# Performance work log

Hardware: AMD Instinct MI355X
Metric: run time of the kernel (lower is better)

Reference implementation:

```python
import jax, jax.numpy as jnp
import numpy as np

N = 50000          # num nodes
E = 800000         # num edges (avg degree 16)
R = 8              # num relations
IN = 128
H0 = 256
H1 = 64


def _w(key, shape, fan_in):
    return jax.random.normal(key, shape, dtype=jnp.float32) * (1.0 / np.sqrt(fan_in))


def setup_inputs() -> dict:
    key = jax.random.key(0)
    ks = jax.random.split(key, 16)
    x = jax.random.normal(ks[0], (N, IN), dtype=jnp.float32)
    edge_index = jax.random.randint(ks[1], (2, E), 0, N, dtype=jnp.int64)
    edge_type = jax.random.randint(ks[2], (E,), 0, R, dtype=jnp.int64)
    return {
        "x": x,
        "edge_index": edge_index,
        "edge_type": edge_type,
        # RGCNConv params: per-relation weights [R, in, out], root weight [in, out], bias [out]
        "W1": _w(ks[3], (R, IN, H0), IN), "root1": _w(ks[4], (IN, H0), IN), "b1": jnp.zeros((H0,), jnp.float32),
        "W2": _w(ks[5], (R, H0, H0), H0), "root2": _w(ks[6], (H0, H0), H0), "b2": jnp.zeros((H0,), jnp.float32),
        "W3": _w(ks[7], (R, H0, H0), H0), "root3": _w(ks[8], (H0, H0), H0), "b3": jnp.zeros((H0,), jnp.float32),
        "W4": _w(ks[9], (R, H0, H1), H0), "root4": _w(ks[10], (H0, H1), H0), "b4": jnp.zeros((H1,), jnp.float32),
    }


def rgcn_layer(x, edge_index, edge_type, W, root, bias):
    """PyG RGCNConv: out_i = x_i @ root + sum_r (1/|N_r(i)|) sum_{j in N_r(i)} x_j @ W_r + bias.
    Aggregation is linear, so aggregate source features per (relation, dst) first,
    then apply the R small GEMMs — avoids per-edge [E, out] message materialization."""
    src, dst = edge_index[0], edge_index[1]
    seg = edge_type * N + dst                      # combined (relation, dst) segment id
    nseg = R * N
    agg = jax.ops.segment_sum(x[src], seg, num_segments=nseg)          # [R*N, in]
    cnt = jax.ops.segment_sum(jnp.ones((seg.shape[0],), x.dtype), seg, num_segments=nseg)
    agg = agg / jnp.maximum(cnt, 1.0)[:, None]                          # mean per (r, i)
    agg = agg.reshape(R, N, x.shape[1])                                 # [R, N, in]
    return jnp.einsum('rni,rio->no', agg, W) + x @ root + bias


def reference(x, edge_index, edge_type, W1, root1, b1, W2, root2, b2, W3, root3, b3, W4, root4, b4):
    h = jax.nn.relu(rgcn_layer(x, edge_index, edge_type, W1, root1, b1))
    h = jax.nn.relu(rgcn_layer(h, edge_index, edge_type, W2, root2, b2))
    h = jax.nn.relu(rgcn_layer(h, edge_index, edge_type, W3, root3, b3))
    return rgcn_layer(h, edge_index, edge_type, W4, root4, b4)
```

## Files before the change

### kernel.cpp

```cpp
#include <hip/hip_runtime.h>

#define N_NODES 50000
#define N_PAD   50048
#define N_EDGES 800000
#define N_REL   8
#define NSEG    (N_REL * N_NODES)
#define SCAN_NB 391
#define NSTRIPE 391
#define SPX     49

typedef short bf16x8 __attribute__((ext_vector_type(8)));
typedef float f32x4  __attribute__((ext_vector_type(4)));

__device__ __forceinline__ ushort f2bf(float f) {
    union { float f; unsigned u; } c; c.f = f;
    unsigned u = c.u + 0x7fffu + ((c.u >> 16) & 1u);
    return (ushort)(u >> 16);
}
__device__ __forceinline__ void add8(float* s, uint4 v) {
    unsigned u[4] = {v.x, v.y, v.z, v.w};
    #pragma unroll
    for (int k = 0; k < 4; ++k) {
        s[2 * k]     += __uint_as_float(u[k] << 16);
        s[2 * k + 1] += __uint_as_float(u[k] & 0xffff0000u);
    }
}
__device__ __forceinline__ void fma8(float* s, uint4 v, float w) {
    unsigned u[4] = {v.x, v.y, v.z, v.w};
    #pragma unroll
    for (int k = 0; k < 4; ++k) {
        s[2 * k]     = fmaf(__uint_as_float(u[k] << 16),        w, s[2 * k]);
        s[2 * k + 1] = fmaf(__uint_as_float(u[k] & 0xffff0000u), w, s[2 * k + 1]);
    }
}
__device__ __forceinline__ void async16(const ushort* g, ushort* l) {
    __builtin_amdgcn_global_load_lds((const __attribute__((address_space(1))) void*)g,
                                     (__attribute__((address_space(3))) void*)l, 16, 0, 0);
}


__global__ void count_edges(const int* __restrict__ dst, const int* __restrict__ et,
                            int* __restrict__ cnt) {
    int e = blockIdx.x * 256 + threadIdx.x;
    if (e < N_EDGES) atomicAdd(&cnt[dst[e] * N_REL + et[e]], 1);
}

__global__ __launch_bounds__(256) void scan_pass1(const int* __restrict__ cnt,
                                                  int* __restrict__ sums) {
    __shared__ int sc[256];
    int b = blockIdx.x, t = threadIdx.x;
    int base = b * 1024 + t * 4;
    int v = 0;
    #pragma unroll
    for (int i = 0; i < 4; ++i) { int idx = base + i; if (idx < NSEG) v += cnt[idx]; }
    sc[t] = v; __syncthreads();
    for (int off = 1; off < 256; off <<= 1) {
        int x = (t >= off) ? sc[t - off] : 0;
        __syncthreads(); sc[t] += x; __syncthreads();
    }
    if (t == 255) sums[b] = sc[255];
}

__global__ __launch_bounds__(512) void scan_pass2(int* __restrict__ sums, int nb) {
    __shared__ int sc[512];
    int t = threadIdx.x;
    int v = (t < nb) ? sums[t] : 0;
    sc[t] = v; __syncthreads();
    for (int off = 1; off < 512; off <<= 1) {
        int x = (t >= off) ? sc[t - off] : 0;
        __syncthreads(); sc[t] += x; __syncthreads();
    }
    if (t < nb) sums[t] = sc[t] - v;
}

__global__ __launch_bounds__(256) void scan_pass3(const int* __restrict__ cnt,
                                                  const int* __restrict__ sums,
                                                  int* __restrict__ row_ptr) {
    __shared__ int sc[256];
    int b = blockIdx.x, t = threadIdx.x;
    int base = b * 1024 + t * 4;
    int e[4]; int v = 0;
    #pragma unroll
    for (int i = 0; i < 4; ++i) { int idx = base + i; e[i] = (idx < NSEG) ? cnt[idx] : 0; v += e[i]; }
    sc[t] = v; __syncthreads();
    for (int off = 1; off < 256; off <<= 1) {
        int x = (t >= off) ? sc[t - off] : 0;
        __syncthreads(); sc[t] += x; __syncthreads();
    }
    int run = sums[b] + (sc[t] - v);
    #pragma unroll
    for (int i = 0; i < 4; ++i) {
        int idx = base + i;
        if (idx < NSEG) row_ptr[idx] = run;
        run += e[i];
    }
    if (b == 0 && t == 0) row_ptr[NSEG] = N_EDGES;
}

__global__ void place_edges(const int* __restrict__ src, const int* __restrict__ dst,
                            const int* __restrict__ et, const int* __restrict__ row_ptr,
                            int* __restrict__ cnt, int* __restrict__ sorted) {
    int e = blockIdx.x * 256 + threadIdx.x;
    if (e >= N_EDGES) return;
    int r = et[e];
    int key = dst[e] * N_REL + r;
    int old = atomicSub(&cnt[key], 1);
    int r0 = row_ptr[key];
    int c = row_ptr[key + 1] - r0;
    sorted[r0 + old - 1] = src[e] | (r << 17) | (c << 20);
}


__global__ void convert_weights(const float* __restrict__ W, const float* __restrict__ root,
                                ushort* __restrict__ BT, int K, int O, int NPAD) {
    int idx = blockIdx.x * 256 + threadIdx.x;
    if (idx >= NPAD * K) return;
    int col = idx / K, i = idx % K;
    float v = 0.0f;
    if (col < N_REL * O) {
        int r = col / O, o = col % O;
        v = W[((size_t)r * K + i) * O + o];
    } else if (col < (N_REL + 1) * O) {
        v = root[(size_t)i * O + (col - N_REL * O)];
    }
    BT[idx] = f2bf(v);
}

__global__ void f32_to_bf16(const float* __restrict__ in, ushort* __restrict__ out, int n4) {
    int i = blockIdx.x * 256 + threadIdx.x;
    if (i >= n4) return;
    float4 v = ((const float4*)in)[i];
    ushort4 s; s.x = f2bf(v.x); s.y = f2bf(v.y); s.z = f2bf(v.z); s.w = f2bf(v.w);
    ((ushort4*)out)[i] = s;
}

template<int K, int CTS, int NW>
__global__ __launch_bounds__(256)
void gemm_mfma(const ushort* __restrict__ A, const ushort* __restrict__ BT,
               ushort* __restrict__ Y) {
    const int f = blockIdx.x;
    const int g = f & 7, m = f >> 3;
    const int y = g + 8 * (m / CTS);
    const int ct = m % CTS;
    if (y >= NSTRIPE) return;
    const int row0 = y * 128;
    const int col0 = ct * 128;

    __shared__ ushort SMEM[8192];
    ushort* As = SMEM;
    ushort* Bs = SMEM + 4096;
    const int t = threadIdx.x;
    const int lane = t & 63;
    const int w = t >> 6;
    const int l16 = lane & 15, q = lane >> 4;
    const int wm = (w & 1) * 64, wn = (w >> 1) * 64;

    const int c0i = w * 64 + lane;
    const int c1i = c0i + 256;
    const size_t ga0 = (size_t)(c0i >> 2) * K + (size_t)(c0i & 3) * 8;
    const size_t ga1 = (size_t)(c1i >> 2) * K + (size_t)(c1i & 3) * 8;
    const ushort* Ab = A + (size_t)row0 * K;
    const ushort* Bb = BT + (size_t)col0 * K;
    ushort* lA0 = &As[w * 512];
    ushort* lA1 = &As[(w + 4) * 512];
    ushort* lB0 = &Bs[w * 512];
    ushort* lB1 = &Bs[(w + 4) * 512];

    f32x4 acc[4][4] = {};

    #pragma unroll
    for (int k0 = 0; k0 < K; k0 += 32) {
        __syncthreads();
        async16(Ab + k0 + ga0, lA0);
        async16(Ab + k0 + ga1, lA1);
        async16(Bb + k0 + ga0, lB0);
        async16(Bb + k0 + ga1, lB1);
        __syncthreads();
        bf16x8 a[4], b[4];
        #pragma unroll
        for (int i = 0; i < 4; ++i) {
            a[i] = *(const bf16x8*)&As[(wm + i * 16 + l16) * 32 + q * 8];
            b[i] = *(const bf16x8*)&Bs[(wn + i * 16 + l16) * 32 + q * 8];
        }
        #pragma unroll
        for (int i = 0; i < 4; ++i)
            #pragma unroll
            for (int j = 0; j < 4; ++j)
                acc[i][j] = __builtin_amdgcn_mfma_f32_16x16x32_bf16(b[j], a[i], acc[i][j], 0, 0, 0);
    }

    #pragma unroll
    for (int i = 0; i < 4; ++i) {
        const size_t rbase = (size_t)(row0 + wm + i * 16 + l16) * NW + col0 + wn + q * 4;
        #pragma unroll
        for (int j = 0; j < 4; ++j) {
            uint2 v;
            v.x = (unsigned)f2bf(acc[i][j][0]) | ((unsigned)f2bf(acc[i][j][1]) << 16);
            v.y = (unsigned)f2bf(acc[i][j][2]) | ((unsigned)f2bf(acc[i][j][3]) << 16);
            *(uint2*)(Y + rbase + j * 16) = v;
        }
    }
}

template<int O>
__global__ __launch_bounds__(256)
void gather_kernel(const ushort* __restrict__ Y, int NW,
                   const int* __restrict__ row_ptr, const int* __restrict__ sorted,
                   const float* __restrict__ bias,
                   float* __restrict__ out_f32, ushort* __restrict__ out_bf16, int relu) {
    constexpr int TPN = O / 8;
    int d = blockIdx.x * (256 / TPN) + threadIdx.x / TPN;
    if (d >= N_NODES) return;
    int c0 = (threadIdx.x % TPN) * 8;
    int p0 = row_ptr[d * N_REL];
    int p1 = row_ptr[d * N_REL + N_REL];
    float sum[8] = {};
    add8(sum, *(const uint4*)(Y + (size_t)d * NW + N_REL * O + c0));
    #pragma unroll
    for (int k = 0; k < 8; ++k) sum[k] += bias[c0 + k];
    const ushort* Yc = Y + c0;
    #define EDGE_LD(sx) (*(const uint4*)(Yc + (size_t)((sx) & 0x1FFFF) * NW + ((((sx) >> 17) & 7) * O)))
    #define EDGE_W(sx)  (1.0f / (float)((unsigned)(sx) >> 20))
    int e = p0;
    for (; e + 4 <= p1; e += 4) {
        int s0 = sorted[e], s1 = sorted[e + 1], s2 = sorted[e + 2], s3 = sorted[e + 3];
        uint4 v0 = EDGE_LD(s0);
        uint4 v1 = EDGE_LD(s1);
        uint4 v2 = EDGE_LD(s2);
        uint4 v3 = EDGE_LD(s3);
        fma8(sum, v0, EDGE_W(s0));
        fma8(sum, v1, EDGE_W(s1));
        fma8(sum, v2, EDGE_W(s2));
        fma8(sum, v3, EDGE_W(s3));
    }
    for (; e < p1; ++e) {
        int s = sorted[e];
        uint4 v = EDGE_LD(s);
        fma8(sum, v, EDGE_W(s));
    }
    #undef EDGE_LD
    #undef EDGE_W
    if (relu) {
        #pragma unroll
        for (int k = 0; k < 8; ++k) sum[k] = fmaxf(sum[k], 0.0f);
    }
    if (out_bf16) {
        ushort o[8];
        #pragma unroll
        for (int k = 0; k < 8; ++k) o[k] = f2bf(sum[k]);
        *(uint4*)(out_bf16 + (size_t)d * O + c0) = *(const uint4*)o;
    } else {
        float* p = out_f32 + (size_t)d * O + c0;
        *(float4*)p = make_float4(sum[0], sum[1], sum[2], sum[3]);
        *(float4*)(p + 4) = make_float4(sum[4], sum[5], sum[6], sum[7]);
    }
}


extern "C" void kernel_launch(void* const* d_in, const int* in_sizes, int n_in,
                              void* d_out, int out_size, void* d_ws, size_t ws_size,
                              hipStream_t stream) {
    const float* x  = (const float*)d_in[0];
    const int*   ei = (const int*)d_in[1];
    const int*   et = (const int*)d_in[2];
    const float* W[4]  = {(const float*)d_in[3], (const float*)d_in[6], (const float*)d_in[9],  (const float*)d_in[12]};
    const float* RT[4] = {(const float*)d_in[4], (const float*)d_in[7], (const float*)d_in[10], (const float*)d_in[13]};
    const float* BI[4] = {(const float*)d_in[5], (const float*)d_in[8], (const float*)d_in[11], (const float*)d_in[14]};
    const int KS[4] = {128, 256, 256, 256};
    const int NP[4] = {2304, 2304, 2304, 640};
    const int* src = ei;
    const int* dst = ei + N_EDGES;

    char* ws = (char*)d_ws;
    size_t off = 0;
    auto take = [&](size_t bytes) -> char* {
        char* p = ws + off;
        off = (off + bytes + 255) & ~(size_t)255;
        return p;
    };
    int* row_ptr    = (int*)take((size_t)(NSEG + 1) * 4);
    int* sorted     = (int*)take((size_t)N_EDGES * 4);
    ushort* BTp[4];
    for (int l = 0; l < 4; ++l) BTp[l] = (ushort*)take((size_t)NP[l] * KS[l] * 2);
    ushort* hb = (ushort*)take((size_t)N_PAD * 256 * 2);
    ushort* Yb = (ushort*)take((size_t)N_PAD * 2304 * 2);
    int* cnt  = (int*)Yb;
    int* sums = (int*)((char*)Yb + (size_t)NSEG * 4);

    hipMemsetAsync(cnt, 0, (size_t)NSEG * 4, stream);
    count_edges<<<(N_EDGES + 255) / 256, 256, 0, stream>>>(dst, et, cnt);
    scan_pass1<<<SCAN_NB, 256, 0, stream>>>(cnt, sums);
    scan_pass2<<<1, 512, 0, stream>>>(sums, SCAN_NB);
    scan_pass3<<<SCAN_NB, 256, 0, stream>>>(cnt, sums, row_ptr);
    place_edges<<<(N_EDGES + 255) / 256, 256, 0, stream>>>(src, dst, et, row_ptr, cnt, sorted);

    for (int l = 0; l < 4; ++l) {
        int n = NP[l] * KS[l];
        convert_weights<<<(n + 255) / 256, 256, 0, stream>>>(W[l], RT[l], BTp[l], KS[l],
                                                             l == 3 ? 64 : 256, NP[l]);
    }

    f32_to_bf16<<<(N_NODES * 128 / 4 + 255) / 256, 256, 0, stream>>>(x, hb, N_NODES * 128 / 4);

    const int G18 = 8 * SPX * 18;
    const int G5  = 8 * SPX * 5;
    gemm_mfma<128, 18, 2304><<<G18, 256, 0, stream>>>(hb, BTp[0], Yb);
    gather_kernel<256><<<dim3((N_NODES + 7) / 8), 256, 0, stream>>>(
        Yb, 2304, row_ptr, sorted, BI[0], nullptr, hb, 1);

    gemm_mfma<256, 18, 2304><<<G18, 256, 0, stream>>>(hb, BTp[1], Yb);
    gather_kernel<256><<<dim3((N_NODES + 7) / 8), 256, 0, stream>>>(
        Yb, 2304, row_ptr, sorted, BI[1], nullptr, hb, 1);

    gemm_mfma<256, 18, 2304><<<G18, 256, 0, stream>>>(hb, BTp[2], Yb);
    gather_kernel<256><<<dim3((N_NODES + 7) / 8), 256, 0, stream>>>(
        Yb, 2304, row_ptr, sorted, BI[2], nullptr, hb, 1);

    gemm_mfma<256, 5, 640><<<G5, 256, 0, stream>>>(hb, BTp[3], Yb);
    gather_kernel<64><<<dim3((N_NODES + 31) / 32), 256, 0, stream>>>(
        Yb, 640, row_ptr, sorted, BI[3], (float*)d_out, nullptr, 0);
}
```

Before: 776.6 us.

## Swizzle GEMM LDS tiles and stage epilogue through LDS for coalesced stores

The GEMM's A/B shared-memory tiles now use an XOR swizzle on the 8-element chunk index, applied to both the global-to-LDS async load offsets and the fragment reads, to cut LDS bank conflicts. The MFMA operand order is swapped, and the epilogue writes each wave's accumulator block transposed into a padded LDS scratch region. It then reads it back in full rows so global stores become 16-byte coalesced writes instead of scattered 8-byte ones. This enlarges shared memory and adds an extra barrier plus LDS round-trip in the epilogue.

Result: faster. 671.0 us (-13.6%).

```diff
diff --git a/kernel.cpp b/kernel.cpp
--- a/kernel.cpp
+++ b/kernel.cpp
@@ -146,7 +146,7 @@
     const int row0 = y * 128;
     const int col0 = ct * 128;
 
-    __shared__ ushort SMEM[8192];
+    __shared__ ushort SMEM[9216];
     ushort* As = SMEM;
     ushort* Bs = SMEM + 4096;
     const int t = threadIdx.x;
@@ -157,14 +157,19 @@
 
     const int c0i = w * 64 + lane;
     const int c1i = c0i + 256;
-    const size_t ga0 = (size_t)(c0i >> 2) * K + (size_t)(c0i & 3) * 8;
-    const size_t ga1 = (size_t)(c1i >> 2) * K + (size_t)(c1i & 3) * 8;
+    const int r0i = c0i >> 2, r1i = c1i >> 2;
+    const int j0i = (c0i & 3) ^ ((r0i >> 1) & 3);
+    const int j1i = (c1i & 3) ^ ((r1i >> 1) & 3);
+    const size_t ga0 = (size_t)r0i * K + (size_t)j0i * 8;
+    const size_t ga1 = (size_t)r1i * K + (size_t)j1i * 8;
     const ushort* Ab = A + (size_t)row0 * K;
     const ushort* Bb = BT + (size_t)col0 * K;
     ushort* lA0 = &As[w * 512];
     ushort* lA1 = &As[(w + 4) * 512];
     ushort* lB0 = &Bs[w * 512];
     ushort* lB1 = &Bs[(w + 4) * 512];
+
+    const int qx = (q ^ ((l16 >> 1) & 3)) * 8;
 
     f32x4 acc[4][4] = {};
 
@@ -179,25 +184,34 @@
         bf16x8 a[4], b[4];
         #pragma unroll
         for (int i = 0; i < 4; ++i) {
-            a[i] = *(const bf16x8*)&As[(wm + i * 16 + l16) * 32 + q * 8];
-            b[i] = *(const bf16x8*)&Bs[(wn + i * 16 + l16) * 32 + q * 8];
+            a[i] = *(const bf16x8*)&As[(wm + i * 16 + l16) * 32 + qx];
+            b[i] = *(const bf16x8*)&Bs[(wn + i * 16 + l16) * 32 + qx];
         }
         #pragma unroll
         for (int i = 0; i < 4; ++i)
             #pragma unroll
             for (int j = 0; j < 4; ++j)
-                acc[i][j] = __builtin_amdgcn_mfma_f32_16x16x32_bf16(b[j], a[i], acc[i][j], 0, 0, 0);
-    }
-
-    #pragma unroll
-    for (int i = 0; i < 4; ++i) {
-        const size_t rbase = (size_t)(row0 + wm + i * 16 + l16) * NW + col0 + wn + q * 4;
-        #pragma unroll
-        for (int j = 0; j < 4; ++j) {
-            uint2 v;
-            v.x = (unsigned)f2bf(acc[i][j][0]) | ((unsigned)f2bf(acc[i][j][1]) << 16);
-            v.y = (unsigned)f2bf(acc[i][j][2]) | ((unsigned)f2bf(acc[i][j][3]) << 16);
-            *(uint2*)(Y + rbase + j * 16) = v;
+                acc[i][j] = __builtin_amdgcn_mfma_f32_16x16x32_bf16(a[i], b[j], acc[i][j], 0, 0, 0);
+    }
+
+    __syncthreads();
+    ushort* Ts = &SMEM[w * 32 * 72];
+    const int rr = lane >> 3;
+    const int cc = (lane & 7) * 8;
+    #pragma unroll
+    for (int half = 0; half < 2; ++half) {
+        #pragma unroll
+        for (int i = 0; i < 2; ++i)
+            #pragma unroll
+            for (int j = 0; j < 4; ++j)
+                #pragma unroll
+                for (int r = 0; r < 4; ++r)
+                    Ts[(i * 16 + q * 4 + r) * 72 + j * 16 + l16] = f2bf(acc[half * 2 + i][j][r]);
+        #pragma unroll
+        for (int p = 0; p < 4; ++p) {
+            int row = p * 8 + rr;
+            uint4 v = *(const uint4*)&Ts[row * 72 + cc];
+            *(uint4*)(Y + (size_t)(row0 + wm + half * 32 + row) * NW + col0 + wn + cc) = v;
         }
     }
 }
```
